# Kernel optimization log

Hardware: AMD Instinct MI355X
Metric: run time of the kernel (lower is better)

The kernel has to match this reference:

```python
import jax, jax.numpy as jnp
import numpy as np

R_SPHERE = 3.0   # bounding_sphere_radius
NEAR = 0.0       # near_distance
FAR = 100.0      # far_distance
SECANT_STEPS = 4 # manifold_secant_steps
EPS = 1e-4
R0 = 1.0         # base radius of analytic manifold field


def setup_inputs() -> dict:
    key = jax.random.key(0)
    ks = jax.random.split(key, 6)
    B, R, L, H = 4, 8192, 4, 64
    rays_o = jax.random.normal(ks[0], (B, R, 3), dtype=jnp.float32) * 0.2  # origins inside sphere
    rd = jax.random.normal(ks[1], (B, R, 3), dtype=jnp.float32)
    rays_d = rd / jnp.linalg.norm(rd, axis=-1, keepdims=True)
    levels = jnp.linspace(0.5, -0.5, L, dtype=jnp.float32)  # manifold_levels parameter
    W1 = jax.random.normal(ks[2], (3, H), dtype=jnp.float32) * 0.3
    b1 = jnp.zeros((H,), dtype=jnp.float32)
    W2 = jax.random.normal(ks[3], (H, 1), dtype=jnp.float32) * 0.1
    b2 = jnp.zeros((1,), dtype=jnp.float32)
    rays_idx = jax.random.randint(ks[4], (B, R), 0, B, dtype=jnp.int64) if jax.config.jax_enable_x64 else jax.random.randint(ks[4], (B, R), 0, B, dtype=jnp.int32)
    mask_gt = jnp.ones((B, R), dtype=bool)
    return {"rays_o": rays_o, "rays_d": rays_d, "levels": levels, "W1": W1, "b1": b1,
            "W2": W2, "b2": b2, "mask_gt": mask_gt, "rays_idx": rays_idx, "num_samples": 64}


def _ray_march(rays_o, rays_d, levels, W1, b1, W2, b2, num_samples):
    B, Rn = rays_o.shape[:2]
    N = B * Rn
    L = levels.shape[0]
    o = rays_o.reshape(N, 3)
    d = rays_d.reshape(N, 3)

    def manifold_fn(x):
        # analytic stand-in for M(x_d, idx): scalar field + validity mask
        h = jnp.tanh(x @ W1 + b1)
        nrm = jnp.linalg.norm(x, axis=-1)
        s = (h @ W2)[..., 0] + b2[0] + (R0 - nrm)
        return s, nrm < R_SPHERE

    # ray-sphere intersection (unit-norm directions assumed, as in source)
    b = jnp.sum(o * d, axis=-1)
    c = jnp.sum(o * o, axis=-1) - R_SPHERE ** 2
    disc = b * b - c
    hit = disc > 0
    sq = jnp.sqrt(jnp.where(hit, disc, 1.0))
    d_near = jnp.maximum(-b - sq, NEAR)
    d_far = jnp.minimum(-b + sq, FAR)
    mask_bound = hit & (d_near < d_far)

    # stratified (uniform) depth samples, (N, S)
    t = jnp.linspace(0.0, 1.0, num_samples, dtype=rays_o.dtype)[None, :]
    ds = d_near[:, None] * (1 - t) + d_far[:, None] * t
    x_d = o[:, None, :] + d[:, None, :] * ds[..., None]  # (N, S, 3)
    scal, m_valid = manifold_fn(x_d)                      # (N, S)

    # --- find_closest_interval ---
    S = num_samples
    dep_f, dep_b = ds[:, :-1], ds[:, 1:]
    sc_f, sc_b = scal[:, :-1], scal[:, 1:]
    m_pair = m_valid[:, :-1] & m_valid[:, 1:]
    l3 = levels[None, :, None]                            # (1, L, 1)
    in_interval = (sc_f[:, None, :] >= l3) & (l3 >= sc_b[:, None, :]) & m_pair[:, None, :]
    rank = jnp.sign(l3 - sc_b[:, None, :]) * jnp.arange(S - 1, 0, -1, dtype=scal.dtype)
    ind_closest = jnp.argmax(rank, axis=2)                # (N, L)
    ind_lowest = jnp.broadcast_to(jnp.argmin(sc_b, axis=1)[:, None], (N, L))
    mask_surface = jnp.any(in_interval, axis=2)
    idx = jnp.where(mask_surface, ind_closest, ind_lowest)
    d_front = jnp.take_along_axis(dep_f, idx, axis=1)
    d_back = jnp.take_along_axis(dep_b, idx, axis=1)
    s_front = jnp.take_along_axis(sc_f, idx, axis=1)
    s_back = jnp.take_along_axis(sc_b, idx, axis=1)

    # --- find_exact_intersection ---
    lr = levels[None, :]                                  # (1, L)
    s_diff = s_front - s_back
    m_vdiff = jnp.abs(s_diff) > EPS
    mask_intersect = (s_front >= lr) & (lr >= s_back)
    mask_secant = mask_intersect & m_vdiff
    s_diff_safe = jnp.where(m_vdiff, s_diff, 1.0)
    d_secant = ((lr - s_back) * d_front + (s_front - lr) * d_back) / s_diff_safe
    d_init = jnp.where(mask_secant, d_secant, d_back)

    # secant refinement (fixed step count; masked full-array updates replace
    # torch's boolean-indexed subset updates with identical math on masked lanes)
    dfs, dbs, sfs, sbs, dcur = d_front, d_back, s_front, s_back, d_init
    for _ in range(SECANT_STEPS):
        x_mid = o[:, None, :] + dcur[..., None] * d[:, None, :]  # (N, L, 3)
        s_mid, mv = manifold_fn(x_mid)
        upf = (s_mid > lr) & mv
        upb = (s_mid < lr) & mv
        dfs = jnp.where(upf, dcur, dfs)
        sfs = jnp.where(upf, s_mid, sfs)
        dbs = jnp.where(upb, dcur, dbs)
        sbs = jnp.where(upb, s_mid, sbs)
        sd = sfs - sbs
        ok = jnp.abs(sd) > EPS
        dcur = jnp.where(ok, ((lr - sbs) * dfs + (sfs - lr) * dbs) / jnp.where(ok, sd, 1.0), dcur)
    d_intersect = jnp.where(mask_secant, dcur, d_init)

    # sort intersections by depth (use_presort=False branch)
    order = jnp.argsort(d_intersect, axis=1)
    d_intersect = jnp.take_along_axis(d_intersect, order, axis=1)
    mask_intersect = jnp.take_along_axis(mask_intersect, order, axis=1)

    dist = jnp.where(mask_bound[:, None], d_intersect, 0.0).reshape(B, Rn, L)
    mask = (mask_intersect & mask_bound[:, None]).reshape(B, Rn, L)
    return dist, mask


def reference(rays_o, rays_d, levels, W1, b1, W2, b2, mask_gt, rays_idx, num_samples):
    # mask_gt / rays_idx are unused in eval mode (use_gt_mask_when_training=False,
    # analytic manifold_fn ignores batch index), kept for signature fidelity.
    return _ray_march(rays_o, rays_d, levels, W1, b1, W2, b2, num_samples)
```

## Files before the change

### kernel.cpp

```cpp
#include <hip/hip_runtime.h>
#include <cstdint>

#define R_SPHEREf 3.0f
#define NEARf 0.0f
#define FARf 100.0f
#define SECANT_STEPS 4
#define EPSf 1e-4f
#define R0f 1.0f
#define Hh 64
#define Lc 4
#define Sn 64

#define C_HI 2.88539004325866699f
#define C_LO 3.8519227871e-08f

__device__ __forceinline__ float fastdiv(float a, float b) {
    float r = __builtin_amdgcn_rcpf(b);
    r = __builtin_fmaf(r, __builtin_fmaf(-b, r, 1.0f), r);
    return a * r;
}

__global__ __launch_bounds__(256) void manifold_render_kernel(
    const float* __restrict__ rays_o, const float* __restrict__ rays_d,
    const float* __restrict__ levels, const float* __restrict__ W1,
    const float* __restrict__ b1, const float* __restrict__ W2,
    const float* __restrict__ b2, float* __restrict__ out, int N)
{
    __shared__ float4 abq[4][Hh];
    __shared__ float Pbuf[4][Hh][33];

    const int tid = threadIdx.x;
    const int wave = tid >> 6;
    const int lane = tid & 63;
    const int r = blockIdx.x * 4 + wave;
    if (r >= N) return;

    const float b2v = b2[0];
    float lvl[Lc];
#pragma unroll
    for (int j = 0; j < Lc; ++j) lvl[j] = levels[j];

    const float ox = rays_o[3 * r], oy = rays_o[3 * r + 1], oz = rays_o[3 * r + 2];
    const float dx = rays_d[3 * r], dy = rays_d[3 * r + 1], dz = rays_d[3 * r + 2];

    const float w1x = W1[lane], w1y = W1[Hh + lane], w1z = W1[2 * Hh + lane];
    const float w2lane = W2[lane];
    const float Ah = __builtin_fmaf(oz, w1z, __builtin_fmaf(oy, w1y,
                     __builtin_fmaf(ox, w1x, b1[lane])));
    const float Bh = __builtin_fmaf(dz, w1z, __builtin_fmaf(dy, w1y, dx * w1x));
    const float A2 = __builtin_fmaf(Ah, C_LO, Ah * C_HI);
    const float B2 = __builtin_fmaf(Bh, C_LO, Bh * C_HI);
    const float zq = -2.0f * w2lane;
    abq[wave][lane] = make_float4(A2, B2, zq, 0.0f);

    float w2sum = w2lane;
#pragma unroll
    for (int m = 1; m < 64; m <<= 1) w2sum += __shfl_xor(w2sum, m);
    const float sbase = w2sum + b2v + R0f;

    const float bq = ox * dx + oy * dy + oz * dz;
    const float cq = ox * ox + oy * oy + oz * oz - R_SPHEREf * R_SPHEREf;
    const float disc = bq * bq - cq;
    const bool hit = disc > 0.0f;
    const float sqv = __builtin_amdgcn_sqrtf(hit ? disc : 1.0f);
    const float d_near = fmaxf(-bq - sqv, NEARf);
    const float d_far  = fminf(-bq + sqv, FARf);
    const bool mask_bound = hit && (d_near < d_far);

    const float delta = (d_far - d_near) * (1.0f / 63.0f);
    const float zs = copysignf(fmaxf(fabsf(zq), 1e-30f), zq);
    float rz = __builtin_amdgcn_rcpf(zs);
    rz = __builtin_fmaf(rz, __builtin_fmaf(-zs, rz, 1.0f), rz);
    const float e0 = __builtin_amdgcn_exp2f(__builtin_fmaf(d_near, B2, A2));
    const float g  = __builtin_amdgcn_exp2f(B2 * delta);
    const float cc = (1.0f - g) * rz;
    float u = __builtin_fmaf(e0, rz, rz);

    float* __restrict__ Pw = &Pbuf[wave][0][0];
    const int sl = lane & 31;
    float accA, accB;

#pragma unroll
    for (int s = 0; s < 32; ++s) {
        Pw[lane * 33 + s] = __builtin_amdgcn_rcpf(u);
        u = __builtin_fmaf(u, g, cc);
    }
    {
        float a0 = 0.f, a1 = 0.f, a2 = 0.f, a3 = 0.f;
#pragma unroll
        for (int h = 0; h < Hh; h += 4) {
            a0 += Pw[(h    ) * 33 + sl];
            a1 += Pw[(h + 1) * 33 + sl];
            a2 += Pw[(h + 2) * 33 + sl];
            a3 += Pw[(h + 3) * 33 + sl];
        }
        accA = (a0 + a1) + (a2 + a3);
    }
    asm volatile("s_waitcnt lgkmcnt(0)" ::: "memory");
#pragma unroll
    for (int s = 0; s < 32; ++s) {
        Pw[lane * 33 + s] = __builtin_amdgcn_rcpf(u);
        u = __builtin_fmaf(u, g, cc);
    }
    {
        float a0 = 0.f, a1 = 0.f, a2 = 0.f, a3 = 0.f;
#pragma unroll
        for (int h = 0; h < Hh; h += 4) {
            a0 += Pw[(h    ) * 33 + sl];
            a1 += Pw[(h + 1) * 33 + sl];
            a2 += Pw[(h + 2) * 33 + sl];
            a3 += Pw[(h + 3) * 33 + sl];
        }
        accB = (a0 + a1) + (a2 + a3);
    }
    const float acc = (lane < 32) ? accA : accB;

    const float t = (float)lane * (1.0f / 63.0f);
    const float dsv = d_near * (1.0f - t) + d_far * t;
    const float x0 = ox + dx * dsv, x1 = oy + dy * dsv, x2 = oz + dz * dsv;
    const float nrm = __builtin_amdgcn_sqrtf(x0 * x0 + x1 * x1 + x2 * x2);
    const float scal = (acc + sbase) - nrm;
    const bool valid = nrm < R_SPHEREf;

    const float scb = __shfl_down(scal, 1);
    const int validn = __shfl_down((int)valid, 1);
    const bool is_int = lane < (Sn - 1);

    float keyv = is_int ? scb : INFINITY;
    int keyi = lane;
#pragma unroll
    for (int m = 1; m < 64; m <<= 1) {
        float ov = __shfl_xor(keyv, m);
        int oi = __shfl_xor(keyi, m);
        if (ov < keyv || (ov == keyv && oi < keyi)) { keyv = ov; keyi = oi; }
    }
    const int ind_lowest = keyi;

    const bool inint_base = is_int && valid && (validn != 0);

    bool mintb[Lc], msec[Lc];
    float dinit[Lc];
    float g_dfs = 0.f, g_dbs = 0.f, g_sfs = 0.f, g_sbs = 0.f, g_dcur = 0.f, g_lr = 0.f;
    const int gl = lane >> 4;

#pragma unroll
    for (int lv = 0; lv < Lc; ++lv) {
        const float l = lvl[lv];
        unsigned long long bP = __ballot(is_int && (scb < l));
        unsigned long long bZ = __ballot(is_int && (scb == l));
        unsigned long long bI = __ballot(inint_base && (scal >= l) && (l >= scb));
        int ind_closest = bP ? __builtin_ctzll(bP)
                             : (bZ ? __builtin_ctzll(bZ) : (Sn - 2));
        bool mask_surface = (bI != 0ULL);
        int idx = mask_surface ? ind_closest : ind_lowest;

        float d_front = __shfl(dsv, idx);
        float d_back  = __shfl(dsv, idx + 1);
        float s_front = __shfl(scal, idx);
        float s_back  = __shfl(scal, idx + 1);

        bool mi = (s_front >= l) && (l >= s_back);
        float sd = s_front - s_back;
        bool vd = fabsf(sd) > EPSf;
        bool ms = mi && vd;
        float d_sec = fastdiv((l - s_back) * d_front + (s_front - l) * d_back,
                              vd ? sd : 1.0f);
        float di = ms ? d_sec : d_back;

        mintb[lv] = mi; msec[lv] = ms; dinit[lv] = di;
        if (gl == lv) {
            g_dfs = d_front; g_dbs = d_back; g_sfs = s_front; g_sbs = s_back;
            g_dcur = di; g_lr = l;
        }
    }

    const float4* __restrict__ ab = &abq[wave][0];
    const int sub = lane & 15;
    float4 sq0 = ab[sub], sq1 = ab[sub + 16], sq2 = ab[sub + 32], sq3 = ab[sub + 48];

#pragma unroll
    for (int it = 0; it < SECANT_STEPS; ++it) {
        float mx0 = ox + g_dcur * dx, mx1 = oy + g_dcur * dy, mx2 = oz + g_dcur * dz;
        float mn = __builtin_amdgcn_sqrtf(mx0 * mx0 + mx1 * mx1 + mx2 * mx2);
        float part;
        {
            float y0 = __builtin_fmaf(g_dcur, sq0.y, sq0.x);
            float y1 = __builtin_fmaf(g_dcur, sq1.y, sq1.x);
            float y2 = __builtin_fmaf(g_dcur, sq2.y, sq2.x);
            float y3 = __builtin_fmaf(g_dcur, sq3.y, sq3.x);
            float r0 = __builtin_amdgcn_rcpf(__builtin_amdgcn_exp2f(y0) + 1.0f);
            float r1 = __builtin_amdgcn_rcpf(__builtin_amdgcn_exp2f(y1) + 1.0f);
            float r2 = __builtin_amdgcn_rcpf(__builtin_amdgcn_exp2f(y2) + 1.0f);
            float r3 = __builtin_amdgcn_rcpf(__builtin_amdgcn_exp2f(y3) + 1.0f);
            part = sq0.z * r0;
            part = __builtin_fmaf(sq1.z, r1, part);
            part = __builtin_fmaf(sq2.z, r2, part);
            part = __builtin_fmaf(sq3.z, r3, part);
        }
#pragma unroll
        for (int m = 1; m < 16; m <<= 1) part += __shfl_xor(part, m, 16);
        float s_mid = (part + sbase) - mn;
        bool mv = mn < R_SPHEREf;
        bool upf = (s_mid > g_lr) && mv;
        bool upb = (s_mid < g_lr) && mv;
        if (upf) { g_dfs = g_dcur; g_sfs = s_mid; }
        if (upb) { g_dbs = g_dcur; g_sbs = s_mid; }
        float sd2 = g_sfs - g_sbs;
        bool ok = fabsf(sd2) > EPSf;
        if (ok) g_dcur = fastdiv((g_lr - g_sbs) * g_dfs + (g_sfs - g_lr) * g_dbs, sd2);
    }

    float v0, v1, v2, v3;
    {
        float dc0 = __shfl(g_dcur, 0);
        float dc1 = __shfl(g_dcur, 16);
        float dc2 = __shfl(g_dcur, 32);
        float dc3 = __shfl(g_dcur, 48);
        v0 = msec[0] ? dc0 : dinit[0];
        v1 = msec[1] ? dc1 : dinit[1];
        v2 = msec[2] ? dc2 : dinit[2];
        v3 = msec[3] ? dc3 : dinit[3];
    }
    int m0 = mintb[0], m1 = mintb[1], m2 = mintb[2], m3 = mintb[3];
    int i0 = 0, i1 = 1, i2 = 2, i3 = 3;

#define CSWAP(va, ia, ma, vb, ib, mb)                                    \
    { bool sw = (vb < va) || (vb == va && ib < ia);                      \
      if (sw) { float tv = va; va = vb; vb = tv;                         \
                int ti = ia; ia = ib; ib = ti;                           \
                int tm = ma; ma = mb; mb = tm; } }
    CSWAP(v0, i0, m0, v1, i1, m1);
    CSWAP(v2, i2, m2, v3, i3, m3);
    CSWAP(v0, i0, m0, v2, i2, m2);
    CSWAP(v1, i1, m1, v3, i3, m3);
    CSWAP(v1, i1, m1, v2, i2, m2);
#undef CSWAP

    const long long NL = (long long)N * Lc;
    if (lane < Lc) {
        float dv = (lane == 0) ? v0 : (lane == 1) ? v1 : (lane == 2) ? v2 : v3;
        out[(long long)r * Lc + lane] = mask_bound ? dv : 0.0f;
    } else if (lane < 2 * Lc) {
        int k = lane - Lc;
        int mm = (k == 0) ? m0 : (k == 1) ? m1 : (k == 2) ? m2 : m3;
        out[NL + (long long)r * Lc + k] = (mm && mask_bound) ? 1.0f : 0.0f;
    }
}

extern "C" void kernel_launch(void* const* d_in, const int* in_sizes, int n_in,
                              void* d_out, int out_size, void* d_ws, size_t ws_size,
                              hipStream_t stream) {
    const float* rays_o = (const float*)d_in[0];
    const float* rays_d = (const float*)d_in[1];
    const float* levels = (const float*)d_in[2];
    const float* W1 = (const float*)d_in[3];
    const float* b1 = (const float*)d_in[4];
    const float* W2 = (const float*)d_in[5];
    const float* b2 = (const float*)d_in[6];
    float* out = (float*)d_out;

    const int N = in_sizes[0] / 3;
    const int blocks = (N + 3) / 4;
    manifold_render_kernel<<<blocks, 256, 0, stream>>>(
        rays_o, rays_d, levels, W1, b1, W2, b2, out, N);
}
```

Baseline: 129.7 us.

## Replace LDS transpose reduction with register-tiled sample/hidden split and fraction merging

The per-sample tanh sum over 64 hidden units used to be computed lane-per-hidden and then transposed through a padded shared-memory buffer. It is now split in registers: each lane handles 8 samples by 8 hidden units, advancing with a geometric recurrence. Reciprocals are merged pairwise into fraction sums so only two rcp calls are needed per 8 terms, and the result is reduced with three cross-lane shuffles. The secant loop likewise merges reciprocals pairwise, and exp2 arguments are clamped to 60 so products of merged denominators do not overflow. This removes the large LDS buffer and its traffic, which may also raise occupancy, at the cost of some precision risk from multiplying denominators together.

Result: faster. 110.1 us (-15.1%).

```diff
diff --git a/kernel.cpp b/kernel.cpp
--- a/kernel.cpp
+++ b/kernel.cpp
@@ -27,7 +27,6 @@
     const float* __restrict__ b2, float* __restrict__ out, int N)
 {
     __shared__ float4 abq[4][Hh];
-    __shared__ float Pbuf[4][Hh][33];
 
     const int tid = threadIdx.x;
     const int wave = tid >> 6;
@@ -42,6 +41,16 @@
 
     const float ox = rays_o[3 * r], oy = rays_o[3 * r + 1], oz = rays_o[3 * r + 2];
     const float dx = rays_d[3 * r], dy = rays_d[3 * r + 1], dz = rays_d[3 * r + 2];
+
+    const float bq = ox * dx + oy * dy + oz * dz;
+    const float cq = ox * ox + oy * oy + oz * oz - R_SPHEREf * R_SPHEREf;
+    const float disc = bq * bq - cq;
+    const bool hit = disc > 0.0f;
+    const float sqv = __builtin_amdgcn_sqrtf(hit ? disc : 1.0f);
+    const float d_near = fmaxf(-bq - sqv, NEARf);
+    const float d_far  = fminf(-bq + sqv, FARf);
+    const bool mask_bound = hit && (d_near < d_far);
+    const float delta = (d_far - d_near) * (1.0f / 63.0f);
 
     const float w1x = W1[lane], w1y = W1[Hh + lane], w1z = W1[2 * Hh + lane];
     const float w2lane = W2[lane];
@@ -51,75 +60,61 @@
     const float A2 = __builtin_fmaf(Ah, C_LO, Ah * C_HI);
     const float B2 = __builtin_fmaf(Bh, C_LO, Bh * C_HI);
     const float zq = -2.0f * w2lane;
-    abq[wave][lane] = make_float4(A2, B2, zq, 0.0f);
-
-    float w2sum = w2lane;
-#pragma unroll
-    for (int m = 1; m < 64; m <<= 1) w2sum += __shfl_xor(w2sum, m);
-    const float sbase = w2sum + b2v + R0f;
-
-    const float bq = ox * dx + oy * dy + oz * dz;
-    const float cq = ox * ox + oy * oy + oz * oz - R_SPHEREf * R_SPHEREf;
-    const float disc = bq * bq - cq;
-    const bool hit = disc > 0.0f;
-    const float sqv = __builtin_amdgcn_sqrtf(hit ? disc : 1.0f);
-    const float d_near = fmaxf(-bq - sqv, NEARf);
-    const float d_far  = fminf(-bq + sqv, FARf);
-    const bool mask_bound = hit && (d_near < d_far);
-
-    const float delta = (d_far - d_near) * (1.0f / 63.0f);
     const float zs = copysignf(fmaxf(fabsf(zq), 1e-30f), zq);
     float rz = __builtin_amdgcn_rcpf(zs);
     rz = __builtin_fmaf(rz, __builtin_fmaf(-zs, rz, 1.0f), rz);
-    const float e0 = __builtin_amdgcn_exp2f(__builtin_fmaf(d_near, B2, A2));
-    const float g  = __builtin_amdgcn_exp2f(B2 * delta);
-    const float cc = (1.0f - g) * rz;
-    float u = __builtin_fmaf(e0, rz, rz);
-
-    float* __restrict__ Pw = &Pbuf[wave][0][0];
-    const int sl = lane & 31;
-    float accA, accB;
-
-#pragma unroll
-    for (int s = 0; s < 32; ++s) {
-        Pw[lane * 33 + s] = __builtin_amdgcn_rcpf(u);
-        u = __builtin_fmaf(u, g, cc);
-    }
-    {
-        float a0 = 0.f, a1 = 0.f, a2 = 0.f, a3 = 0.f;
-#pragma unroll
-        for (int h = 0; h < Hh; h += 4) {
-            a0 += Pw[(h    ) * 33 + sl];
-            a1 += Pw[(h + 1) * 33 + sl];
-            a2 += Pw[(h + 2) * 33 + sl];
-            a3 += Pw[(h + 3) * 33 + sl];
+    const float Gh = __builtin_amdgcn_exp2f(B2 * (8.0f * delta));
+    abq[wave][lane] = make_float4(A2, B2, rz, Gh);
+
+    float w2sum = w2lane;
+#pragma unroll
+    for (int m = 1; m < 64; m <<= 1) w2sum += __shfl_xor(w2sum, m);
+    const float sbase = w2sum + b2v + R0f;
+
+    const int hg = lane >> 3;
+    const int sl = lane & 7;
+    const float dsl = __builtin_fmaf((float)sl, delta, d_near);
+
+    const float4* __restrict__ ab = &abq[wave][0];
+    float v[8], Gr[8], K[8];
+#pragma unroll
+    for (int j = 0; j < 8; ++j) {
+        const float4 q = ab[hg + 8 * j];
+        const float y = fminf(__builtin_fmaf(dsl, q.y, q.x), 60.0f);
+        const float e0 = __builtin_amdgcn_exp2f(y);
+        v[j]  = __builtin_fmaf(e0, q.z, q.z);
+        Gr[j] = q.w;
+        K[j]  = __builtin_fmaf(-q.z, q.w, q.z);
+    }
+
+    float mysum = 0.0f;
+#pragma unroll
+    for (int it = 0; it < 8; ++it) {
+        if (it > 0) {
+#pragma unroll
+            for (int j = 0; j < 8; ++j) v[j] = __builtin_fmaf(v[j], Gr[j], K[j]);
         }
-        accA = (a0 + a1) + (a2 + a3);
-    }
-    asm volatile("s_waitcnt lgkmcnt(0)" ::: "memory");
-#pragma unroll
-    for (int s = 0; s < 32; ++s) {
-        Pw[lane * 33 + s] = __builtin_amdgcn_rcpf(u);
-        u = __builtin_fmaf(u, g, cc);
-    }
-    {
-        float a0 = 0.f, a1 = 0.f, a2 = 0.f, a3 = 0.f;
-#pragma unroll
-        for (int h = 0; h < Hh; h += 4) {
-            a0 += Pw[(h    ) * 33 + sl];
-            a1 += Pw[(h + 1) * 33 + sl];
-            a2 += Pw[(h + 2) * 33 + sl];
-            a3 += Pw[(h + 3) * 33 + sl];
-        }
-        accB = (a0 + a1) + (a2 + a3);
-    }
-    const float acc = (lane < 32) ? accA : accB;
+        const float n01 = v[0] + v[1], d01 = v[0] * v[1];
+        const float n23 = v[2] + v[3], d23 = v[2] * v[3];
+        const float numA = __builtin_fmaf(n23, d01, n01 * d23);
+        const float denA = d01 * d23;
+        const float n45 = v[4] + v[5], d45 = v[4] * v[5];
+        const float n67 = v[6] + v[7], d67 = v[6] * v[7];
+        const float numB = __builtin_fmaf(n67, d45, n45 * d67);
+        const float denB = d45 * d67;
+        float part = numA * __builtin_amdgcn_rcpf(denA);
+        part = __builtin_fmaf(numB, __builtin_amdgcn_rcpf(denB), part);
+        part += __shfl_xor(part, 8);
+        part += __shfl_xor(part, 16);
+        part += __shfl_xor(part, 32);
+        if (it == hg) mysum = part;
+    }
 
     const float t = (float)lane * (1.0f / 63.0f);
     const float dsv = d_near * (1.0f - t) + d_far * t;
     const float x0 = ox + dx * dsv, x1 = oy + dy * dsv, x2 = oz + dz * dsv;
     const float nrm = __builtin_amdgcn_sqrtf(x0 * x0 + x1 * x1 + x2 * x2);
-    const float scal = (acc + sbase) - nrm;
+    const float scal = (mysum + sbase) - nrm;
     const bool valid = nrm < R_SPHEREf;
 
     const float scb = __shfl_down(scal, 1);
@@ -174,7 +169,6 @@
         }
     }
 
-    const float4* __restrict__ ab = &abq[wave][0];
     const int sub = lane & 15;
     float4 sq0 = ab[sub], sq1 = ab[sub + 16], sq2 = ab[sub + 32], sq3 = ab[sub + 48];
 
@@ -184,18 +178,22 @@
         float mn = __builtin_amdgcn_sqrtf(mx0 * mx0 + mx1 * mx1 + mx2 * mx2);
         float part;
         {
-            float y0 = __builtin_fmaf(g_dcur, sq0.y, sq0.x);
-            float y1 = __builtin_fmaf(g_dcur, sq1.y, sq1.x);
-            float y2 = __builtin_fmaf(g_dcur, sq2.y, sq2.x);
-            float y3 = __builtin_fmaf(g_dcur, sq3.y, sq3.x);
-            float r0 = __builtin_amdgcn_rcpf(__builtin_amdgcn_exp2f(y0) + 1.0f);
-            float r1 = __builtin_amdgcn_rcpf(__builtin_amdgcn_exp2f(y1) + 1.0f);
-            float r2 = __builtin_amdgcn_rcpf(__builtin_amdgcn_exp2f(y2) + 1.0f);
-            float r3 = __builtin_amdgcn_rcpf(__builtin_amdgcn_exp2f(y3) + 1.0f);
-            part = sq0.z * r0;
-            part = __builtin_fmaf(sq1.z, r1, part);
-            part = __builtin_fmaf(sq2.z, r2, part);
-            part = __builtin_fmaf(sq3.z, r3, part);
+            float y0 = fminf(__builtin_fmaf(g_dcur, sq0.y, sq0.x), 60.0f);
+            float y1 = fminf(__builtin_fmaf(g_dcur, sq1.y, sq1.x), 60.0f);
+            float y2 = fminf(__builtin_fmaf(g_dcur, sq2.y, sq2.x), 60.0f);
+            float y3 = fminf(__builtin_fmaf(g_dcur, sq3.y, sq3.x), 60.0f);
+            float e0 = __builtin_amdgcn_exp2f(y0);
+            float e1 = __builtin_amdgcn_exp2f(y1);
+            float e2 = __builtin_amdgcn_exp2f(y2);
+            float e3 = __builtin_amdgcn_exp2f(y3);
+            float v0 = __builtin_fmaf(e0, sq0.z, sq0.z);
+            float v1 = __builtin_fmaf(e1, sq1.z, sq1.z);
+            float v2 = __builtin_fmaf(e2, sq2.z, sq2.z);
+            float v3 = __builtin_fmaf(e3, sq3.z, sq3.z);
+            float n01 = v0 + v1, d01 = v0 * v1;
+            float n23 = v2 + v3, d23 = v2 * v3;
+            part = n01 * __builtin_amdgcn_rcpf(d01);
+            part = __builtin_fmaf(n23, __builtin_amdgcn_rcpf(d23), part);
         }
 #pragma unroll
         for (int m = 1; m < 16; m <<= 1) part += __shfl_xor(part, m, 16);
@@ -210,16 +208,16 @@
         if (ok) g_dcur = fastdiv((g_lr - g_sbs) * g_dfs + (g_sfs - g_lr) * g_dbs, sd2);
     }
 
-    float v0, v1, v2, v3;
+    float v0g, v1g, v2g, v3g;
     {
         float dc0 = __shfl(g_dcur, 0);
         float dc1 = __shfl(g_dcur, 16);
         float dc2 = __shfl(g_dcur, 32);
         float dc3 = __shfl(g_dcur, 48);
-        v0 = msec[0] ? dc0 : dinit[0];
-        v1 = msec[1] ? dc1 : dinit[1];
-        v2 = msec[2] ? dc2 : dinit[2];
-        v3 = msec[3] ? dc3 : dinit[3];
+        v0g = msec[0] ? dc0 : dinit[0];
+        v1g = msec[1] ? dc1 : dinit[1];
+        v2g = msec[2] ? dc2 : dinit[2];
+        v3g = msec[3] ? dc3 : dinit[3];
     }
     int m0 = mintb[0], m1 = mintb[1], m2 = mintb[2], m3 = mintb[3];
     int i0 = 0, i1 = 1, i2 = 2, i3 = 3;
@@ -229,16 +227,16 @@
       if (sw) { float tv = va; va = vb; vb = tv;                         \
                 int ti = ia; ia = ib; ib = ti;                           \
                 int tm = ma; ma = mb; mb = tm; } }
-    CSWAP(v0, i0, m0, v1, i1, m1);
-    CSWAP(v2, i2, m2, v3, i3, m3);
-    CSWAP(v0, i0, m0, v2, i2, m2);
-    CSWAP(v1, i1, m1, v3, i3, m3);
-    CSWAP(v1, i1, m1, v2, i2, m2);
+    CSWAP(v0g, i0, m0, v1g, i1, m1);
+    CSWAP(v2g, i2, m2, v3g, i3, m3);
+    CSWAP(v0g, i0, m0, v2g, i2, m2);
+    CSWAP(v1g, i1, m1, v3g, i3, m3);
+    CSWAP(v1g, i1, m1, v2g, i2, m2);
 #undef CSWAP
 
     const long long NL = (long long)N * Lc;
     if (lane < Lc) {
-        float dv = (lane == 0) ? v0 : (lane == 1) ? v1 : (lane == 2) ? v2 : v3;
+        float dv = (lane == 0) ? v0g : (lane == 1) ? v1g : (lane == 2) ? v2g : v3g;
         out[(long long)r * Lc + lane] = mask_bound ? dv : 0.0f;
     } else if (lane < 2 * Lc) {
         int k = lane - Lc;
```
